# Performance work log

Hardware: AMD Instinct MI355X
Metric: run time of the kernel (lower is better)

The kernel has to match this reference:

```python
import jax, jax.numpy as jnp
import numpy as np

EPS = 1e-5
L = 8      # n_layers
H = 1024   # n_hidden
F_IN = 26  # input features
B = 65536  # batch


def layer_norm(x, gamma, beta):
    m = jnp.mean(x, axis=-1, keepdims=True)
    v = jnp.mean((x - m) ** 2, axis=-1, keepdims=True)
    return (x - m) * jax.lax.rsqrt(v + EPS) * gamma + beta


def setup_inputs() -> dict:
    key = jax.random.key(0)
    ks = jax.random.split(key, 12)
    s_in = 1.0 / np.sqrt(F_IN)
    s_h = 1.0 / np.sqrt(H)
    return {
        "x": jax.random.normal(ks[0], (B, F_IN), jnp.float32),
        "st_gamma": jnp.ones((F_IN,), jnp.float32),
        "st_beta": jnp.zeros((F_IN,), jnp.float32),
        "st_w": jax.random.uniform(ks[1], (H, F_IN), jnp.float32, -s_in, s_in),
        "st_b": jax.random.uniform(ks[2], (H,), jnp.float32, -s_in, s_in),
        "blk_gamma": jnp.ones((L, H), jnp.float32),
        "blk_beta": jnp.zeros((L, H), jnp.float32),
        "blk_w": jax.random.uniform(ks[3], (L, H, H), jnp.float32, -s_h, s_h),
        "blk_b": jax.random.uniform(ks[4], (L, H), jnp.float32, -s_h, s_h),
        "last_gamma": jnp.ones((H,), jnp.float32),
        "last_beta": jnp.zeros((H,), jnp.float32),
        "last_w": jax.random.uniform(ks[5], (1, H), jnp.float32, -s_h, s_h),
        "last_b": jax.random.uniform(ks[6], (1,), jnp.float32, -s_h, s_h),
    }


def reference(x, st_gamma, st_beta, st_w, st_b,
              blk_gamma, blk_beta, blk_w, blk_b,
              last_gamma, last_beta, last_w, last_b):
    # Stem: LN(26) -> Linear(26->H) -> ReLU (dropout = identity in eval)
    h = jax.nn.relu(layer_norm(x, st_gamma, st_beta) @ st_w.T + st_b)

    # n_layers blocks: LN -> Linear(H->H) -> ReLU, scanned over stacked params
    def body(h, params):
        g, b, w, bb = params
        h = jax.nn.relu(layer_norm(h, g, b) @ w.T + bb)
        return h, None

    h, _ = jax.lax.scan(body, h, (blk_gamma, blk_beta, blk_w, blk_b))

    # Head: LN -> Linear(H->1) -> sigmoid
    h = layer_norm(h, last_gamma, last_beta)
    out = jax.nn.sigmoid(h @ last_w.T + last_b)  # [B, 1]
    return out
```

## Files before the change

kernel.cpp:

```cpp
#include <hip/hip_runtime.h>
#include <hip/hip_bf16.h>
#include <stdint.h>


typedef __attribute__((ext_vector_type(8))) _Float16 f16x8;
typedef __attribute__((ext_vector_type(4))) float f32x4;

#define EPSLN 1e-5f
#define HDIM 1024

__device__ __forceinline__ void gload16(const void* g, void* l) {
  __builtin_amdgcn_global_load_lds(
      (const __attribute__((address_space(1))) unsigned int*)g,
      (__attribute__((address_space(3))) unsigned int*)l, 16, 0, 0);
}

__global__ __launch_bounds__(256) void zero_f32(float* __restrict__ p, int n) {
  int i = blockIdx.x * 256 + threadIdx.x;
  if (i < n) p[i] = 0.f;
}

__global__ __launch_bounds__(256) void fold_blk(
    const float* __restrict__ bg, const float* __restrict__ bb,
    const float* __restrict__ bw, const float* __restrict__ bbias,
    _Float16* __restrict__ Wf, float* __restrict__ bfold, float* __restrict__ Sfold) {
  int lo = blockIdx.x;
  int layer = lo >> 10;
  const float* wrow = bw + (size_t)lo * HDIM;
  const float* g = bg + (size_t)layer * HDIM;
  const float* be = bb + (size_t)layer * HDIM;
  _Float16* wout = Wf + (size_t)lo * HDIM;
  int t = threadIdx.x;
  float s = 0.f, acb = 0.f;
  for (int i = t; i < HDIM; i += 256) {
    float wv = wrow[i];
    _Float16 wp = (_Float16)(wv * g[i]);
    wout[i] = wp;
    s += (float)wp;
    acb += be[i] * wv;
  }
#pragma unroll
  for (int off = 1; off < 64; off <<= 1) { s += __shfl_xor(s, off); acb += __shfl_xor(acb, off); }
  __shared__ float rs[4], rb[4];
  int l = t & 63, w = t >> 6;
  if (l == 0) { rs[w] = s; rb[w] = acb; }
  __syncthreads();
  if (t == 0) {
    Sfold[lo] = rs[0] + rs[1] + rs[2] + rs[3];
    bfold[lo] = bbias[lo] + rb[0] + rb[1] + rb[2] + rb[3];
  }
}

__global__ __launch_bounds__(256) void fold_head(
    const float* __restrict__ lg, const float* __restrict__ lb,
    const float* __restrict__ lw, const float* __restrict__ lbias,
    float* __restrict__ headW, float* __restrict__ headAux) {
  int t = threadIdx.x;
  float s = 0.f, acb = 0.f;
  for (int i = t; i < HDIM; i += 256) {
    float wp = lw[i] * lg[i];
    headW[i] = wp;
    s += wp;
    acb += lb[i] * lw[i];
  }
#pragma unroll
  for (int off = 1; off < 64; off <<= 1) { s += __shfl_xor(s, off); acb += __shfl_xor(acb, off); }
  __shared__ float rs[4], rb[4];
  int l = t & 63, w = t >> 6;
  if (l == 0) { rs[w] = s; rb[w] = acb; }
  __syncthreads();
  if (t == 0) {
    headAux[0] = rs[0] + rs[1] + rs[2] + rs[3];
    headAux[1] = lbias[0] + rb[0] + rb[1] + rb[2] + rb[3];
  }
}

__global__ __launch_bounds__(256) void fold_stem(const float* __restrict__ stw,
                                                 _Float16* __restrict__ Wst) {
  int idx = blockIdx.x * 256 + threadIdx.x;
  int o = idx >> 6, j = idx & 63;
  int i = (((j >> 3) ^ (o & 7)) << 3) + (j & 7);
  Wst[idx] = (i < 26) ? (_Float16)stw[o * 26 + i] : (_Float16)0.f;
}

__global__ __launch_bounds__(256) void stem_gemm(
    const float* __restrict__ x, const float* __restrict__ stg, const float* __restrict__ stb,
    const _Float16* __restrict__ Wst, const float* __restrict__ stbias,
    _Float16* __restrict__ hout, float* __restrict__ stats_out, int rowBase) {
  __shared__ float xin[128 * 26];
  __shared__ _Float16 As[128 * 64];
  __shared__ _Float16 Bs[128 * 64];
  const int t = threadIdx.x;
  const int l = t & 63;
  const int w = t >> 6;
  const int wm = w >> 1, wn = w & 1;
  const int brow = blockIdx.x * 128;
  const int bcol = blockIdx.y * 128;

  const _Float16* gb = Wst + (size_t)(bcol + (t >> 3)) * 64 + (t & 7) * 8;
  char* lB = (char*)Bs + (size_t)w * 1024;
#pragma unroll
  for (int q = 0; q < 4; ++q) gload16(gb + (size_t)q * 32 * 64, lB + q * 4096);

  const float* src = x + ((size_t)rowBase + brow) * 26;
  for (int i = t; i < 128 * 26; i += 256) xin[i] = src[i];
  __syncthreads();

  if (t < 128) {
    float m = 0.f;
#pragma unroll
    for (int i = 0; i < 26; ++i) m += xin[t * 26 + i];
    m *= (1.f / 26.f);
    float v = 0.f;
#pragma unroll
    for (int i = 0; i < 26; ++i) { float d = xin[t * 26 + i] - m; v += d * d; }
    float rstd = rsqrtf(v * (1.f / 26.f) + EPSLN);
    _Float16 tmp[32];
#pragma unroll
    for (int i = 0; i < 26; ++i)
      tmp[i] = (_Float16)((xin[t * 26 + i] - m) * rstd * stg[i] + stb[i]);
#pragma unroll
    for (int i = 26; i < 32; ++i) tmp[i] = (_Float16)0.f;
    char* arow = (char*)As + t * 128;
#pragma unroll
    for (int c = 0; c < 4; ++c) {
      f16x8 vv;
#pragma unroll
      for (int j = 0; j < 8; ++j) vv[j] = tmp[c * 8 + j];
      *(f16x8*)(arow + ((c ^ (t & 7)) << 4)) = vv;
    }
    f16x8 vz = (f16x8)(_Float16)0.f;
#pragma unroll
    for (int c = 4; c < 8; ++c) *(f16x8*)(arow + ((c ^ (t & 7)) << 4)) = vz;
  }
  __syncthreads();

  f32x4 acc[4][4];
#pragma unroll
  for (int i = 0; i < 4; ++i)
#pragma unroll
    for (int j = 0; j < 4; ++j) acc[i][j] = (f32x4){0.f, 0.f, 0.f, 0.f};

#pragma unroll
  for (int ks = 0; ks < 2; ++ks) {
    const int cx = ((ks * 4 + (l >> 4)) ^ (l & 7)) << 4;
    f16x8 af[4], bfr[4];
#pragma unroll
    for (int m = 0; m < 4; ++m)
      af[m] = *(const f16x8*)((const char*)As + (wm * 64 + m * 16 + (l & 15)) * 128 + cx);
#pragma unroll
    for (int n = 0; n < 4; ++n)
      bfr[n] = *(const f16x8*)((const char*)Bs + (wn * 64 + n * 16 + (l & 15)) * 128 + cx);
#pragma unroll
    for (int m = 0; m < 4; ++m)
#pragma unroll
      for (int n = 0; n < 4; ++n)
        acc[m][n] = __builtin_amdgcn_mfma_f32_16x16x32_f16(af[m], bfr[n], acc[m][n], 0, 0, 0);
  }

  __syncthreads();
  float* sred = (float*)xin;
  if (t < 256) sred[t] = 0.f;
  __syncthreads();

  float Bf[4];
#pragma unroll
  for (int n = 0; n < 4; ++n) Bf[n] = stbias[bcol + wn * 64 + n * 16 + (l & 15)];
#pragma unroll
  for (int m = 0; m < 4; ++m) {
#pragma unroll
    for (int rg = 0; rg < 4; ++rg) {
      int rloc = wm * 64 + m * 16 + (l >> 4) * 4 + rg;
      int lrow = brow + rloc;
      float ps = 0.f, psq = 0.f;
#pragma unroll
      for (int n = 0; n < 4; ++n) {
        int col = bcol + wn * 64 + n * 16 + (l & 15);
        float vv = fmaxf(acc[m][n][rg] + Bf[n], 0.f);
        hout[(size_t)lrow * HDIM + col] = (_Float16)vv;
        ps += vv; psq += vv * vv;
      }
#pragma unroll
      for (int off = 1; off < 16; off <<= 1) {
        ps += __shfl_xor(ps, off);
        psq += __shfl_xor(psq, off);
      }
      if ((l & 15) == 0) {
        atomicAdd(&sred[rloc * 2 + 0], ps);
        atomicAdd(&sred[rloc * 2 + 1], psq);
      }
    }
  }
  __syncthreads();
  if (t < 256) atomicAdd(&stats_out[(size_t)(brow + (t >> 1)) * 2 + (t & 1)], sred[t]);
}

__global__ __launch_bounds__(256, 2) void layer_gemm(
    const _Float16* __restrict__ hin, const float* __restrict__ stats_in,
    const _Float16* __restrict__ W, const float* __restrict__ bfold,
    const float* __restrict__ Sfold, _Float16* __restrict__ hout,
    float* __restrict__ stats_out) {
  __shared__ __align__(128) char smem[2 * 24576];
  const int t = threadIdx.x;
  const int l = t & 63;
  const int w = t >> 6;
  const int wn = w;
  int bid = blockIdx.x;
  {
    int nb = gridDim.x;
    if ((nb & 7) == 0) { int cpx = nb >> 3; bid = (bid & 7) * cpx + (bid >> 3); }
  }
  const int brow = (bid >> 2) * 128;
  const int bcol = (bid & 3) * 256;

  f32x4 acc[8][4];
#pragma unroll
  for (int i = 0; i < 8; ++i)
#pragma unroll
    for (int j = 0; j < 4; ++j) acc[i][j] = (f32x4){0.f, 0.f, 0.f, 0.f};

  const int cswz = (t & 3) ^ ((t >> 3) & 3);
  const _Float16* gA = hin + (size_t)(brow + (t >> 2)) * HDIM + cswz * 8;
  const _Float16* gB = W + (size_t)(bcol + (t >> 2)) * HDIM + cswz * 8;
  const int dstw = w << 10;

  auto stage = [&](int kt) {
    char* base = smem + (kt & 1) * 24576;
    char* dA = base + dstw;
    char* dB = base + 8192 + dstw;
    const _Float16* sA = gA + kt * 32;
    const _Float16* sB = gB + kt * 32;
    gload16(sA, dA);
    gload16(sA + (size_t)64 * HDIM, dA + 4096);
    gload16(sB, dB);
    gload16(sB + (size_t)64 * HDIM, dB + 4096);
    gload16(sB + (size_t)128 * HDIM, dB + 8192);
    gload16(sB + (size_t)192 * HDIM, dB + 12288);
  };

  const int rl = l & 15;
  const int cx = (((l >> 4) ^ ((rl >> 1) & 3)) << 4);
  const int arow0 = rl * 64 + cx;
  const int brow0 = 8192 + (wn * 64 + rl) * 64 + cx;

#define TILE_END()                                   \
  do {                                               \
    __builtin_amdgcn_sched_barrier(0);               \
    asm volatile("s_waitcnt vmcnt(0)" ::: "memory"); \
    __builtin_amdgcn_s_barrier();                    \
    __builtin_amdgcn_sched_barrier(0);               \
  } while (0)

  auto tile = [&](int kt, bool st) {
    if (st) stage(kt + 1);
    const char* bc = smem + (kt & 1) * 24576;
    f16x8 bf[4], af[8];
#pragma unroll
    for (int n = 0; n < 4; ++n) bf[n] = *(const f16x8*)(bc + brow0 + n * 1024);
#pragma unroll
    for (int m = 0; m < 8; ++m) af[m] = *(const f16x8*)(bc + arow0 + m * 1024);
    __builtin_amdgcn_s_setprio(1);
#pragma unroll
    for (int m = 0; m < 8; ++m)
#pragma unroll
      for (int n = 0; n < 4; ++n)
        acc[m][n] = __builtin_amdgcn_mfma_f32_16x16x32_f16(af[m], bf[n], acc[m][n], 0, 0, 0);
    __builtin_amdgcn_s_setprio(0);
    TILE_END();
  };

  stage(0);
  TILE_END();

#pragma unroll 1
  for (int kt = 0; kt < 31; ++kt) tile(kt, true);
  tile(31, false);
#undef TILE_END

  float* sred = (float*)smem;
  sred[t] = 0.f;
  __syncthreads();

  float Sf[4], Bf2[4];
#pragma unroll
  for (int n = 0; n < 4; ++n) {
    int col = bcol + wn * 64 + n * 16 + rl;
    Sf[n] = Sfold[col];
    Bf2[n] = bfold[col];
  }
#pragma unroll
  for (int m = 0; m < 8; ++m) {
#pragma unroll
    for (int rg = 0; rg < 4; ++rg) {
      int rloc = m * 16 + (l >> 4) * 4 + rg;
      int grow = brow + rloc;
      float sum = stats_in[(size_t)grow * 2 + 0];
      float sumsq = stats_in[(size_t)grow * 2 + 1];
      float mean = sum * (1.f / 1024.f);
      float rstd = rsqrtf(sumsq * (1.f / 1024.f) - mean * mean + EPSLN);
      float ps = 0.f, psq = 0.f;
#pragma unroll
      for (int n = 0; n < 4; ++n) {
        int col = bcol + wn * 64 + n * 16 + rl;
        float vv = rstd * (acc[m][n][rg] - mean * Sf[n]) + Bf2[n];
        vv = fmaxf(vv, 0.f);
        hout[(size_t)grow * HDIM + col] = (_Float16)vv;
        ps += vv; psq += vv * vv;
      }
#pragma unroll
      for (int off2 = 1; off2 < 16; off2 <<= 1) {
        ps += __shfl_xor(ps, off2);
        psq += __shfl_xor(psq, off2);
      }
      if (rl == 0) {
        atomicAdd(&sred[rloc * 2 + 0], ps);
        atomicAdd(&sred[rloc * 2 + 1], psq);
      }
    }
  }
  __syncthreads();
  atomicAdd(&stats_out[(size_t)(brow + (t >> 1)) * 2 + (t & 1)], sred[t]);
}

__global__ __launch_bounds__(512) void head_kernel(
    const _Float16* __restrict__ h8, const float* __restrict__ stats8,
    const float* __restrict__ headW, const float* __restrict__ headAux,
    float* __restrict__ out, int rowBase) {
  int t = threadIdx.x, l = t & 63, w = t >> 6;
  int lrow = blockIdx.x * 8 + w;
  const f16x8* hp = (const f16x8*)(h8 + (size_t)lrow * HDIM) + l * 2;
  f16x8 v0 = hp[0], v1 = hp[1];
  float acc = 0.f;
#pragma unroll
  for (int j = 0; j < 8; ++j) acc += (float)v0[j] * headW[l * 16 + j];
#pragma unroll
  for (int j = 0; j < 8; ++j) acc += (float)v1[j] * headW[l * 16 + 8 + j];
#pragma unroll
  for (int off = 1; off < 64; off <<= 1) acc += __shfl_xor(acc, off);
  if (l == 0) {
    float sum = stats8[lrow * 2 + 0], sumsq = stats8[lrow * 2 + 1];
    float mean = sum * (1.f / 1024.f);
    float rstd = rsqrtf(sumsq * (1.f / 1024.f) - mean * mean + EPSLN);
    float z = rstd * (acc - mean * headAux[0]) + headAux[1];
    out[rowBase + lrow] = 1.f / (1.f + expf(-z));
  }
}

extern "C" void kernel_launch(void* const* d_in, const int* in_sizes, int n_in,
                              void* d_out, int out_size, void* d_ws, size_t ws_size,
                              hipStream_t stream) {
  const float* x      = (const float*)d_in[0];
  const float* stg    = (const float*)d_in[1];
  const float* stb    = (const float*)d_in[2];
  const float* stw    = (const float*)d_in[3];
  const float* stbias = (const float*)d_in[4];
  const float* bg     = (const float*)d_in[5];
  const float* bb     = (const float*)d_in[6];
  const float* bw     = (const float*)d_in[7];
  const float* bbias  = (const float*)d_in[8];
  const float* lg     = (const float*)d_in[9];
  const float* lb     = (const float*)d_in[10];
  const float* lw     = (const float*)d_in[11];
  const float* lbias  = (const float*)d_in[12];
  float* out = (float*)d_out;
  const int B = 65536;
  const int L = 8;

  char* ws = (char*)d_ws;
  size_t off = 0;
  auto carve = [&](size_t bytes) -> char* {
    char* p = ws + off;
    off = (off + bytes + 255) & ~(size_t)255;
    return p;
  };
  _Float16* Wf   = (_Float16*)carve((size_t)L * HDIM * HDIM * 2);
  float* bfold   = (float*)carve((size_t)L * HDIM * 4);
  float* Sfold   = (float*)carve((size_t)L * HDIM * 4);
  float* headW   = (float*)carve((size_t)HDIM * 4);
  float* headAux = (float*)carve(256);
  _Float16* Wst  = (_Float16*)carve((size_t)HDIM * 64 * 2);
  size_t fixed = off;

  int R = B;
  while (R > 256) {
    size_t need = fixed + 2 * ((size_t)R * HDIM * 2 + 256) + ((size_t)9 * R * 2 * 4 + 256);
    if (need <= ws_size) break;
    R >>= 1;
  }
  _Float16* hA = (_Float16*)carve((size_t)R * HDIM * 2);
  _Float16* hB = (_Float16*)carve((size_t)R * HDIM * 2);
  float* stats = (float*)carve((size_t)9 * R * 2 * 4);

  fold_blk<<<L * HDIM, 256, 0, stream>>>(bg, bb, bw, bbias, Wf, bfold, Sfold);
  fold_head<<<1, 256, 0, stream>>>(lg, lb, lw, lbias, headW, headAux);
  fold_stem<<<HDIM * 64 / 256, 256, 0, stream>>>(stw, Wst);

  const int nstats = 9 * R * 2;
  for (int c = 0; c < B / R; ++c) {
    int rowBase = c * R;
    zero_f32<<<(nstats + 255) / 256, 256, 0, stream>>>(stats, nstats);
    {
      dim3 grid(R / 128, 8);
      stem_gemm<<<grid, 256, 0, stream>>>(x, stg, stb, Wst, stbias, hA, stats, rowBase);
    }
    _Float16* cur = hA;
    _Float16* nxt = hB;
    for (int lyr = 0; lyr < L; ++lyr) {
      int nb = (R / 128) * 4;
      layer_gemm<<<nb, 256, 0, stream>>>(
          cur, stats + (size_t)lyr * R * 2, Wf + (size_t)lyr * HDIM * HDIM,
          bfold + lyr * HDIM, Sfold + lyr * HDIM, nxt, stats + (size_t)(lyr + 1) * R * 2);
      _Float16* tmp = cur; cur = nxt; nxt = tmp;
    }
    head_kernel<<<R / 8, 512, 0, stream>>>(cur, stats + (size_t)8 * R * 2, headW, headAux, out, rowBase);
  }
}
```

Before: 1.481 ms.

## Load weight B-fragments directly from global into registers, bypassing LDS

The layer GEMM no longer stages the 256-column weight tile through shared memory. Each wave loads its own B fragments straight from global memory into double-buffered registers, while only the activation tile still goes through LDS. This cuts LDS footprint and traffic per block and removes the LDS reads for B. In exchange it raises register pressure and makes the uncoalesced per-lane global loads of W (each lane reading 16B from a different row) depend on L2 bandwidth and latency, with manual vmcnt accounting that must stay correct.

```diff
diff --git a/kernel.cpp b/kernel.cpp
--- a/kernel.cpp
+++ b/kernel.cpp
@@ -200,7 +200,7 @@
     const _Float16* __restrict__ W, const float* __restrict__ bfold,
     const float* __restrict__ Sfold, _Float16* __restrict__ hout,
     float* __restrict__ stats_out) {
-  __shared__ __align__(128) char smem[2 * 24576];
+  __shared__ __align__(128) char smem[2 * 8192];
   const int t = threadIdx.x;
   const int l = t & 63;
   const int w = t >> 6;
@@ -221,61 +221,96 @@
 
   const int cswz = (t & 3) ^ ((t >> 3) & 3);
   const _Float16* gA = hin + (size_t)(brow + (t >> 2)) * HDIM + cswz * 8;
-  const _Float16* gB = W + (size_t)(bcol + (t >> 2)) * HDIM + cswz * 8;
   const int dstw = w << 10;
 
-  auto stage = [&](int kt) {
-    char* base = smem + (kt & 1) * 24576;
-    char* dA = base + dstw;
-    char* dB = base + 8192 + dstw;
+  auto stageA = [&](int kt) {
+    char* dA = smem + (kt & 1) * 8192 + dstw;
     const _Float16* sA = gA + kt * 32;
-    const _Float16* sB = gB + kt * 32;
     gload16(sA, dA);
     gload16(sA + (size_t)64 * HDIM, dA + 4096);
-    gload16(sB, dB);
-    gload16(sB + (size_t)64 * HDIM, dB + 4096);
-    gload16(sB + (size_t)128 * HDIM, dB + 8192);
-    gload16(sB + (size_t)192 * HDIM, dB + 12288);
   };
+
+  const _Float16* gBf = W + (size_t)(bcol + wn * 64 + (l & 15)) * HDIM + (l >> 4) * 8;
 
   const int rl = l & 15;
   const int cx = (((l >> 4) ^ ((rl >> 1) & 3)) << 4);
   const int arow0 = rl * 64 + cx;
-  const int brow0 = 8192 + (wn * 64 + rl) * 64 + cx;
-
-#define TILE_END()                                   \
-  do {                                               \
-    __builtin_amdgcn_sched_barrier(0);               \
-    asm volatile("s_waitcnt vmcnt(0)" ::: "memory"); \
-    __builtin_amdgcn_s_barrier();                    \
-    __builtin_amdgcn_sched_barrier(0);               \
+
+  f16x8 bf0[4], bf1[4];
+
+#define LOADB(kt, dst)                                                        \
+  do {                                                                        \
+    _Pragma("unroll") for (int n = 0; n < 4; ++n)                             \
+        dst[n] = *(const f16x8*)(gBf + (size_t)n * 16 * HDIM + (kt) * 32);    \
   } while (0)
-
-  auto tile = [&](int kt, bool st) {
-    if (st) stage(kt + 1);
-    const char* bc = smem + (kt & 1) * 24576;
-    f16x8 bf[4], af[8];
-#pragma unroll
-    for (int n = 0; n < 4; ++n) bf[n] = *(const f16x8*)(bc + brow0 + n * 1024);
-#pragma unroll
-    for (int m = 0; m < 8; ++m) af[m] = *(const f16x8*)(bc + arow0 + m * 1024);
-    __builtin_amdgcn_s_setprio(1);
-#pragma unroll
-    for (int m = 0; m < 8; ++m)
-#pragma unroll
-      for (int n = 0; n < 4; ++n)
-        acc[m][n] = __builtin_amdgcn_mfma_f32_16x16x32_f16(af[m], bf[n], acc[m][n], 0, 0, 0);
-    __builtin_amdgcn_s_setprio(0);
-    TILE_END();
-  };
-
-  stage(0);
-  TILE_END();
+#define DS_AF(bufkt)                                                          \
+  do {                                                                        \
+    const char* bc = smem + ((bufkt) & 1) * 8192;                             \
+    _Pragma("unroll") for (int m = 0; m < 8; ++m)                             \
+        af[m] = *(const f16x8*)(bc + arow0 + m * 1024);                       \
+  } while (0)
+#define MFMA32(src)                                                           \
+  do {                                                                        \
+    __builtin_amdgcn_s_setprio(1);                                            \
+    _Pragma("unroll") for (int m = 0; m < 8; ++m)                             \
+        _Pragma("unroll") for (int n = 0; n < 4; ++n)                         \
+            acc[m][n] = __builtin_amdgcn_mfma_f32_16x16x32_f16(af[m], src[n], \
+                                                               acc[m][n], 0, 0, 0); \
+    __builtin_amdgcn_s_setprio(0);                                            \
+  } while (0)
+#define WAIT_PRE(N)                                                           \
+  do {                                                                        \
+    asm volatile("s_waitcnt vmcnt(" #N ") lgkmcnt(0)" ::: "memory");          \
+    __builtin_amdgcn_sched_barrier(0);                                        \
+  } while (0)
+#define BOUNDARY()                                                            \
+  do {                                                                        \
+    __builtin_amdgcn_sched_barrier(0);                                        \
+    asm volatile("s_waitcnt vmcnt(4)" ::: "memory");                          \
+    __builtin_amdgcn_s_barrier();                                             \
+    __builtin_amdgcn_sched_barrier(0);                                        \
+  } while (0)
+
+  f16x8 af[8];
+
+  stageA(0);
+  LOADB(0, bf0);
+  asm volatile("s_waitcnt vmcnt(4)" ::: "memory");
+  __builtin_amdgcn_s_barrier();
+  __builtin_amdgcn_sched_barrier(0);
 
 #pragma unroll 1
-  for (int kt = 0; kt < 31; ++kt) tile(kt, true);
-  tile(31, false);
-#undef TILE_END
+  for (int kt2 = 0; kt2 < 15; ++kt2) {
+    const int kt = kt2 * 2;
+    stageA(kt + 1);
+    LOADB(kt + 1, bf1);
+    DS_AF(kt);
+    WAIT_PRE(6);
+    MFMA32(bf0);
+    BOUNDARY();
+    stageA(kt + 2);
+    LOADB(kt + 2, bf0);
+    DS_AF(kt + 1);
+    WAIT_PRE(6);
+    MFMA32(bf1);
+    BOUNDARY();
+  }
+  stageA(31);
+  LOADB(31, bf1);
+  DS_AF(30);
+  WAIT_PRE(6);
+  MFMA32(bf0);
+  BOUNDARY();
+  DS_AF(31);
+  WAIT_PRE(0);
+  MFMA32(bf1);
+  __syncthreads();
+
+#undef LOADB
+#undef DS_AF
+#undef MFMA32
+#undef WAIT_PRE
+#undef BOUNDARY
 
   float* sred = (float*)smem;
   sred[t] = 0.f;
```

New measurement: 1.776 ms. +19.9%, slower.
